# Optimization experiments

Hardware: AMD Instinct MI355X
Metric: run time of the kernel (lower is better)

The kernel has to match this reference:

```python
import jax, jax.numpy as jnp
import numpy as np


def _gelu(x):
    # torch nn.GELU default = exact erf form
    return jax.nn.gelu(x, approximate=False)


def setup_inputs() -> dict:
    key = jax.random.key(0)
    ks = jax.random.split(key, 10)
    B, C, S, L, Din, Dout = 32, 4, 256, 256, 256, 256
    return {
        "features": jax.random.normal(ks[0], (B, C, S, Din), jnp.float32),
        "features_mean": jax.random.normal(ks[1], (B, S, L), jnp.float32),
        "W1": jax.random.normal(ks[2], (1, 16), jnp.float32) * 0.5,
        "b1": jax.random.normal(ks[3], (16,), jnp.float32) * 0.1,
        "W2": jax.random.normal(ks[4], (16, 8), jnp.float32) * 0.25,
        "b2": jax.random.normal(ks[5], (8,), jnp.float32) * 0.1,
        "W3": jax.random.normal(ks[6], (8, 2), jnp.float32) * 0.35,
        "b3": jax.random.normal(ks[7], (2,), jnp.float32) * 0.1,
        "Wl": jax.random.normal(ks[8], (Din, Dout), jnp.float32) * (1.0 / np.sqrt(Din)),
        "bl": jax.random.normal(ks[9], (Dout,), jnp.float32) * 0.02,
    }


def reference(features, features_mean, W1, b1, W2, b2, W3, b3, Wl, bl):
    B, S, L = features_mean.shape
    # pairwise correlations -> [B, S*S, 1]
    corr = jnp.einsum('bsl,btl->bst', features_mean, features_mean).reshape(B, S * S, 1)
    # tiny pointwise MLP 1->16->8->2 with GELU, then log-softmax
    h = _gelu(corr @ W1 + b1)
    h = _gelu(h @ W2 + b2)
    logits = jax.nn.log_softmax(h @ W3 + b3, axis=-1)  # [B, S*S, 2]
    # gumbel-softmax, hard=True, tau=1 (straight-through; forward value is one-hot)
    u = jax.random.uniform(jax.random.key(42), logits.shape, logits.dtype, 1e-10, 1.0)
    g = -jnp.log(-jnp.log(u))
    y_soft = jax.nn.softmax(logits + g, axis=-1)
    y_hard = jax.nn.one_hot(jnp.argmax(y_soft, axis=-1), 2, dtype=y_soft.dtype)
    y = jax.lax.stop_gradient(y_hard - y_soft) + y_soft
    adj = y[..., 0].reshape(B, S, S)
    # mix in identity: a + (1 - a) * I (forces self-loops)
    eye = jnp.eye(S, dtype=adj.dtype)
    adj = adj + (1.0 - adj) * eye
    # degree (row) normalization
    adj = adj * (1.0 / jnp.sum(adj, axis=-1, keepdims=True))
    # propagate: [B,1,S,S] @ [B,C,S,Din]
    x = jnp.einsum('bst,bctd->bcsd', adj, features)
    return x @ Wl + bl
```

## Files before the change

### kernel.cpp

```cpp
#include <hip/hip_runtime.h>
#include <stdint.h>


#define TBL_INTERVALS 131072
#define TBL_MIN -128.0f
#define TBL_SCALE 512.0f
#define WL_CAP 131072u

typedef __attribute__((ext_vector_type(8))) short short8v;
typedef __attribute__((ext_vector_type(4))) short short4v;
typedef __attribute__((ext_vector_type(4))) float float4v;

__device__ __forceinline__ void threefry2x32(uint32_t x0, uint32_t x1,
                                             uint32_t& o0, uint32_t& o1) {
  const uint32_t ks0 = 0u;
  const uint32_t ks1 = 42u;
  const uint32_t ks2 = 0x1BD11BDAu ^ ks0 ^ ks1;
  const uint32_t ks[3] = {ks0, ks1, ks2};
  const uint32_t rot[2][4] = {{13u, 15u, 26u, 6u}, {17u, 29u, 16u, 24u}};
  x0 += ks0;
  x1 += ks1;
#pragma unroll
  for (int i = 0; i < 5; ++i) {
#pragma unroll
    for (int j = 0; j < 4; ++j) {
      const uint32_t r = rot[i & 1][j];
      x0 += x1;
      x1 = (x1 << r) | (x1 >> (32u - r));
      x1 ^= x0;
    }
    x0 += ks[(i + 1) % 3];
    x1 += ks[(i + 2) % 3] + (uint32_t)(i + 1);
  }
  o0 = x0;
  o1 = x1;
}

__device__ __forceinline__ float uniform_at(uint32_t j) {
  uint32_t o0, o1;
  threefry2x32(0u, j, o0, o1);
  const uint32_t bits = o0 ^ o1;
  uint32_t fb = (bits >> 9) | 0x3F800000u;
  float frac = __uint_as_float(fb) - 1.0f;
  return fmaxf(frac + 1e-10f, 1e-10f);
}

__device__ __forceinline__ double gumbel64_at(uint32_t j) {
  double t = -log((double)uniform_at(j));
  return -log(t);
}

__device__ __forceinline__ float gumbel32_at(uint32_t j) {
  float t = -logf(uniform_at(j));
  return -logf(t);
}

__device__ __forceinline__ double gelu_d(double x) {
  return 0.5 * x * (1.0 + erf(x * 0.70710678118654752440));
}

__device__ __forceinline__ float gelu_f(float x) {
  return 0.5f * x * (1.0f + erff(x * 0.70710678f));
}

__device__ __forceinline__ float mlp32(float corr, const float* __restrict__ W1,
                                       const float* __restrict__ b1,
                                       const float* __restrict__ W2,
                                       const float* __restrict__ b2,
                                       const float* __restrict__ W3,
                                       const float* __restrict__ b3) {
  float h1[16];
#pragma unroll
  for (int u = 0; u < 16; ++u) h1[u] = gelu_f(fmaf(corr, W1[u], b1[u]));
  float h2[8];
#pragma unroll
  for (int v = 0; v < 8; ++v) {
    float x = b2[v];
#pragma unroll
    for (int u = 0; u < 16; ++u) x = fmaf(h1[u], W2[u * 8 + v], x);
    h2[v] = gelu_f(x);
  }
  float l0 = b3[0], l1 = b3[1];
#pragma unroll
  for (int v = 0; v < 8; ++v) {
    l0 = fmaf(h2[v], W3[v * 2 + 0], l0);
    l1 = fmaf(h2[v], W3[v * 2 + 1], l1);
  }
  return l0 - l1;
}

__device__ __forceinline__ void split_bf16(float x, short& h, short& l) {
  uint32_t u = __float_as_uint(x);
  uint32_t hr = (u + 0x7FFFu + ((u >> 16) & 1u)) >> 16;
  float hf = __uint_as_float(hr << 16);
  float lo = x - hf;
  uint32_t v = __float_as_uint(lo);
  uint32_t lr = (v + 0x7FFFu + ((v >> 16) & 1u)) >> 16;
  h = (short)hr;
  l = (short)lr;
}

__device__ __forceinline__ short bf16_exact(float x) {
  return (short)(__float_as_uint(x) >> 16);
}

__global__ __launch_bounds__(256) void build_table_kernel(
    const float* __restrict__ W1, const float* __restrict__ b1,
    const float* __restrict__ W2, const float* __restrict__ b2,
    const float* __restrict__ W3, const float* __restrict__ b3,
    float* __restrict__ tbl) {
  const int i = blockIdx.x * 256 + threadIdx.x;
  if (i > TBL_INTERVALS) return;
  const float x = TBL_MIN + (float)i * (1.0f / TBL_SCALE);
  tbl[i] = mlp32(x, W1, b1, W2, b2, W3, b3);
}

__global__ void init_counter_kernel(uint32_t* __restrict__ c) { c[0] = 0u; }

__global__ __launch_bounds__(256) void corr_mfma_kernel(
    const float* __restrict__ fm, float* __restrict__ corr) {
  const int b = blockIdx.z;
  const float* base = fm + (size_t)b * 65536;
  const int row0 = blockIdx.y * 128;
  const int col0 = blockIdx.x * 128;

  __shared__ short Ah[128][40];
  __shared__ short Al[128][40];
  __shared__ short Bh[128][40];
  __shared__ short Bl[128][40];

  const int tid = threadIdx.x;
  const int w = tid >> 6;
  const int wr = (w >> 1) * 64;
  const int wc = (w & 1) * 64;
  const int lane = tid & 63;
  const int fcol = lane & 15;
  const int kg = lane >> 4;

  const int am = tid >> 1;
  const int ak = (tid & 1) * 16;

  float4v acc[4][4];
#pragma unroll
  for (int i = 0; i < 4; ++i)
#pragma unroll
    for (int j = 0; j < 4; ++j) acc[i][j] = (float4v)(0.0f);

  for (int k0 = 0; k0 < 256; k0 += 32) {
    float4 av[4], bv[4];
#pragma unroll
    for (int q = 0; q < 4; ++q) {
      av[q] = *(const float4*)(base + (size_t)(row0 + am) * 256 + k0 + ak + q * 4);
      bv[q] = *(const float4*)(base + (size_t)(col0 + am) * 256 + k0 + ak + q * 4);
    }

    __syncthreads();

    {
      short h[16], l[16];
#pragma unroll
      for (int q = 0; q < 4; ++q) {
        split_bf16(av[q].x, h[q * 4 + 0], l[q * 4 + 0]);
        split_bf16(av[q].y, h[q * 4 + 1], l[q * 4 + 1]);
        split_bf16(av[q].z, h[q * 4 + 2], l[q * 4 + 2]);
        split_bf16(av[q].w, h[q * 4 + 3], l[q * 4 + 3]);
      }
      *(short8v*)&Ah[am][ak] = *(short8v*)&h[0];
      *(short8v*)&Ah[am][ak + 8] = *(short8v*)&h[8];
      *(short8v*)&Al[am][ak] = *(short8v*)&l[0];
      *(short8v*)&Al[am][ak + 8] = *(short8v*)&l[8];
#pragma unroll
      for (int q = 0; q < 4; ++q) {
        split_bf16(bv[q].x, h[q * 4 + 0], l[q * 4 + 0]);
        split_bf16(bv[q].y, h[q * 4 + 1], l[q * 4 + 1]);
        split_bf16(bv[q].z, h[q * 4 + 2], l[q * 4 + 2]);
        split_bf16(bv[q].w, h[q * 4 + 3], l[q * 4 + 3]);
      }
      *(short8v*)&Bh[am][ak] = *(short8v*)&h[0];
      *(short8v*)&Bh[am][ak + 8] = *(short8v*)&h[8];
      *(short8v*)&Bl[am][ak] = *(short8v*)&l[0];
      *(short8v*)&Bl[am][ak + 8] = *(short8v*)&l[8];
    }
    __syncthreads();

    short8v afh[4], afl[4], bfh[4], bfl[4];
#pragma unroll
    for (int im = 0; im < 4; ++im) {
      afh[im] = *(const short8v*)&Ah[wr + im * 16 + fcol][kg * 8];
      afl[im] = *(const short8v*)&Al[wr + im * 16 + fcol][kg * 8];
    }
#pragma unroll
    for (int in = 0; in < 4; ++in) {
      bfh[in] = *(const short8v*)&Bh[wc + in * 16 + fcol][kg * 8];
      bfl[in] = *(const short8v*)&Bl[wc + in * 16 + fcol][kg * 8];
    }
#pragma unroll
    for (int im = 0; im < 4; ++im)
#pragma unroll
      for (int in = 0; in < 4; ++in) {
        acc[im][in] = __builtin_amdgcn_mfma_f32_16x16x32_bf16(
            afh[im], bfh[in], acc[im][in], 0, 0, 0);
        acc[im][in] = __builtin_amdgcn_mfma_f32_16x16x32_bf16(
            afh[im], bfl[in], acc[im][in], 0, 0, 0);
        acc[im][in] = __builtin_amdgcn_mfma_f32_16x16x32_bf16(
            afl[im], bfh[in], acc[im][in], 0, 0, 0);
        acc[im][in] = __builtin_amdgcn_mfma_f32_16x16x32_bf16(
            afl[im], bfl[in], acc[im][in], 0, 0, 0);
      }
  }

  float* Cb = corr + (size_t)b * 65536;
#pragma unroll
  for (int in = 0; in < 4; ++in) {
    const int col = col0 + wc + in * 16 + fcol;
#pragma unroll
    for (int im = 0; im < 4; ++im) {
      const int rbase = row0 + wr + im * 16 + kg * 4;
#pragma unroll
      for (int r = 0; r < 4; ++r)
        Cb[(size_t)(rbase + r) * 256 + col] = acc[im][in][r];
    }
  }
}

__global__ __launch_bounds__(256) void decide_fast_kernel(
    const float* __restrict__ corr, const float* __restrict__ tbl,
    float* __restrict__ adj_bin, uint32_t* __restrict__ counter,
    uint32_t* __restrict__ worklist) {
  const uint32_t flat = blockIdx.x * 256u + threadIdx.x;
  const int t = flat & 255;
  const int s = (flat >> 8) & 255;

  float a = 1.0f;
  bool pend = false;
  if (t != s) {
    const float cf = corr[flat];
    if (fabsf(cf) >= 127.0f) {
      pend = true;
      a = 0.0f;
    } else {
      const float xf = (cf - TBL_MIN) * TBL_SCALE;
      const int i = (int)xf;
      const float fr = xf - (float)i;
      const float t0v = tbl[i];
      const float t1v = tbl[i + 1];
      const float dt = t1v - t0v;
      const float dphi = fmaf(fr, dt, t0v);

      const float g0 = gumbel32_at(2u * flat);
      const float g1 = gumbel32_at(2u * flat + 1u);
      const float d = dphi - (g1 - g0);
      const float thr = fmaf(fabsf(dt), 0.3072f, 4e-4f);
      if (fabsf(d) >= thr) {
        a = (d >= 0.0f) ? 1.0f : 0.0f;
      } else {
        pend = true;
        a = 0.0f;
      }
    }
  }
  if (pend) {
    const uint32_t idx = atomicAdd(counter, 1u);
    if (idx < WL_CAP) worklist[idx] = flat;
  }
  adj_bin[flat] = a;
}

__global__ __launch_bounds__(256) void decide_exact_kernel(
    const float* __restrict__ fm, const uint32_t* __restrict__ counter,
    const uint32_t* __restrict__ worklist,
    const float* __restrict__ W1, const float* __restrict__ b1,
    const float* __restrict__ W2, const float* __restrict__ b2,
    const float* __restrict__ W3, const float* __restrict__ b3,
    float* __restrict__ adj_bin) {
  const uint32_t n = min(counter[0], WL_CAP);
  const uint32_t waveId = (blockIdx.x * 256u + threadIdx.x) >> 6;
  const uint32_t nWaves = (gridDim.x * 256u) >> 6;
  const int lane = threadIdx.x & 63;

  for (uint32_t it = waveId; it < n; it += nWaves) {
    const uint32_t flat = worklist[it];
    const uint32_t bb = flat >> 16;
    const uint32_t ss = (flat >> 8) & 255u;
    const uint32_t tt = flat & 255u;

    const float* S = fm + ((size_t)bb * 256 + ss) * 256;
    const float* T = fm + ((size_t)bb * 256 + tt) * 256;
    double p = 0.0;
#pragma unroll
    for (int q = 0; q < 4; ++q) {
      const int k = lane + q * 64;
      p += (double)S[k] * (double)T[k];
    }
#pragma unroll
    for (int off = 32; off; off >>= 1) p += __shfl_xor(p, off);
    const double acc = p;

    const double ga = gumbel64_at(2u * flat + (uint32_t)(lane & 1));

    const int u = lane & 15;
    const double h1 = gelu_d(acc * (double)W1[u] + (double)b1[u]);

    const int v = lane & 7;
    double sv = (double)b2[v];
#pragma unroll
    for (int uu = 0; uu < 16; ++uu) {
      const double h1u = __shfl(h1, uu);
      sv += h1u * (double)W2[uu * 8 + v];
    }
    const double h2 = gelu_d(sv);

    double l0 = (double)b3[0], l1 = (double)b3[1];
#pragma unroll
    for (int vv = 0; vv < 8; ++vv) {
      const double h2v = __shfl(h2, vv);
      l0 += h2v * (double)W3[vv * 2 + 0];
      l1 += h2v * (double)W3[vv * 2 + 1];
    }

    const double G0 = __shfl(ga, 0);
    const double G1 = __shfl(ga, 1);
    if (lane == 0) adj_bin[flat] = (l0 + G0 >= l1 + G1) ? 1.0f : 0.0f;
  }
}

__global__ __launch_bounds__(256) void rowscale_kernel(
    const float* __restrict__ adj_bin, float* __restrict__ rs) {
  const int row = blockIdx.x * 4 + (threadIdx.x >> 6);
  const int lane = threadIdx.x & 63;
  float4 v = ((const float4*)(adj_bin + (size_t)row * 256))[lane];
  float sum = v.x + v.y + v.z + v.w;
#pragma unroll
  for (int off = 32; off; off >>= 1) sum += __shfl_xor(sum, off);
  if (lane == 0) rs[row] = 1.0f / sum;
}

__global__ __launch_bounds__(256) void gemm_binA_kernel(
    const float* __restrict__ A, const float* __restrict__ B,
    const float* __restrict__ rs, float* __restrict__ C) {
  const int z = blockIdx.z;
  const float* Ab = A + (size_t)(z / 4) * 65536;
  const float* Bb = B + (size_t)z * 65536;
  const float* rsb = rs + (size_t)(z / 4) * 256;
  float* Cb = C + (size_t)z * 65536;

  const int row0 = blockIdx.y * 128;
  const int col0 = blockIdx.x * 128;

  __shared__ short Ah[128][40];
  __shared__ short Bh[128][40];
  __shared__ short Bl[128][40];

  const int tid = threadIdx.x;
  const int w = tid >> 6;
  const int wr = (w >> 1) * 64;
  const int wc = (w & 1) * 64;
  const int lane = tid & 63;
  const int fcol = lane & 15;
  const int kg = lane >> 4;

  const int am = tid >> 1;
  const int ak = (tid & 1) * 16;
  const int nq = (tid & 31) * 4;
  const int kb = (tid >> 5) * 4;

  float4v acc[4][4];
#pragma unroll
  for (int i = 0; i < 4; ++i)
#pragma unroll
    for (int j = 0; j < 4; ++j) acc[i][j] = (float4v)(0.0f);

  for (int k0 = 0; k0 < 256; k0 += 32) {
    float4 av[4];
#pragma unroll
    for (int q = 0; q < 4; ++q)
      av[q] = *(const float4*)(Ab + (size_t)(row0 + am) * 256 + k0 + ak + q * 4);
    float4 bv[4];
#pragma unroll
    for (int j = 0; j < 4; ++j)
      bv[j] = *(const float4*)(Bb + (size_t)(k0 + kb + j) * 256 + col0 + nq);

    __syncthreads();

    {
      short h[16];
#pragma unroll
      for (int q = 0; q < 4; ++q) {
        h[q * 4 + 0] = bf16_exact(av[q].x);
        h[q * 4 + 1] = bf16_exact(av[q].y);
        h[q * 4 + 2] = bf16_exact(av[q].z);
        h[q * 4 + 3] = bf16_exact(av[q].w);
      }
      *(short8v*)&Ah[am][ak] = *(short8v*)&h[0];
      *(short8v*)&Ah[am][ak + 8] = *(short8v*)&h[8];
    }
    {
      const float bm[4][4] = {{bv[0].x, bv[1].x, bv[2].x, bv[3].x},
                              {bv[0].y, bv[1].y, bv[2].y, bv[3].y},
                              {bv[0].z, bv[1].z, bv[2].z, bv[3].z},
                              {bv[0].w, bv[1].w, bv[2].w, bv[3].w}};
#pragma unroll
      for (int i = 0; i < 4; ++i) {
        short h[4], l[4];
#pragma unroll
        for (int j = 0; j < 4; ++j) split_bf16(bm[i][j], h[j], l[j]);
        *(short4v*)&Bh[nq + i][kb] = *(short4v*)&h[0];
        *(short4v*)&Bl[nq + i][kb] = *(short4v*)&l[0];
      }
    }
    __syncthreads();

    short8v afh[4], bfh[4], bfl[4];
#pragma unroll
    for (int im = 0; im < 4; ++im)
      afh[im] = *(const short8v*)&Ah[wr + im * 16 + fcol][kg * 8];
#pragma unroll
    for (int in = 0; in < 4; ++in) {
      bfh[in] = *(const short8v*)&Bh[wc + in * 16 + fcol][kg * 8];
      bfl[in] = *(const short8v*)&Bl[wc + in * 16 + fcol][kg * 8];
    }
#pragma unroll
    for (int im = 0; im < 4; ++im)
#pragma unroll
      for (int in = 0; in < 4; ++in) {
        acc[im][in] = __builtin_amdgcn_mfma_f32_16x16x32_bf16(
            afh[im], bfh[in], acc[im][in], 0, 0, 0);
        acc[im][in] = __builtin_amdgcn_mfma_f32_16x16x32_bf16(
            afh[im], bfl[in], acc[im][in], 0, 0, 0);
      }
  }

#pragma unroll
  for (int im = 0; im < 4; ++im) {
    const int rbase = row0 + wr + im * 16 + kg * 4;
    float rsv[4];
#pragma unroll
    for (int r = 0; r < 4; ++r) rsv[r] = rsb[rbase + r];
#pragma unroll
    for (int in = 0; in < 4; ++in) {
      const int col = col0 + wc + in * 16 + fcol;
#pragma unroll
      for (int r = 0; r < 4; ++r)
        Cb[(size_t)(rbase + r) * 256 + col] = acc[im][in][r] * rsv[r];
    }
  }
}

__global__ __launch_bounds__(256) void gemm_mfma_kernel(
    const float* __restrict__ A, const float* __restrict__ B,
    const float* __restrict__ bias, float* __restrict__ C) {
  const int z = blockIdx.z;
  const float* Ab = A + (size_t)z * 65536;
  const float* Bb = B;
  float* Cb = C + (size_t)z * 65536;

  const int row0 = blockIdx.y * 128;
  const int col0 = blockIdx.x * 128;

  __shared__ short Ah[128][40];
  __shared__ short Al[128][40];
  __shared__ short Bh[128][40];
  __shared__ short Bl[128][40];

  const int tid = threadIdx.x;
  const int w = tid >> 6;
  const int wr = (w >> 1) * 64;
  const int wc = (w & 1) * 64;
  const int lane = tid & 63;
  const int fcol = lane & 15;
  const int kg = lane >> 4;

  const int am = tid >> 1;
  const int ak = (tid & 1) * 16;
  const int nq = (tid & 31) * 4;
  const int kb = (tid >> 5) * 4;

  float4v acc[4][4];
#pragma unroll
  for (int i = 0; i < 4; ++i)
#pragma unroll
    for (int j = 0; j < 4; ++j) acc[i][j] = (float4v)(0.0f);

  for (int k0 = 0; k0 < 256; k0 += 32) {
    float4 av[4];
#pragma unroll
    for (int q = 0; q < 4; ++q)
      av[q] = *(const float4*)(Ab + (size_t)(row0 + am) * 256 + k0 + ak + q * 4);
    float4 bv[4];
#pragma unroll
    for (int j = 0; j < 4; ++j)
      bv[j] = *(const float4*)(Bb + (size_t)(k0 + kb + j) * 256 + col0 + nq);

    __syncthreads();

    {
      short h[16], l[16];
#pragma unroll
      for (int q = 0; q < 4; ++q) {
        split_bf16(av[q].x, h[q * 4 + 0], l[q * 4 + 0]);
        split_bf16(av[q].y, h[q * 4 + 1], l[q * 4 + 1]);
        split_bf16(av[q].z, h[q * 4 + 2], l[q * 4 + 2]);
        split_bf16(av[q].w, h[q * 4 + 3], l[q * 4 + 3]);
      }
      *(short8v*)&Ah[am][ak] = *(short8v*)&h[0];
      *(short8v*)&Ah[am][ak + 8] = *(short8v*)&h[8];
      *(short8v*)&Al[am][ak] = *(short8v*)&l[0];
      *(short8v*)&Al[am][ak + 8] = *(short8v*)&l[8];
    }
    {
      const float bm[4][4] = {{bv[0].x, bv[1].x, bv[2].x, bv[3].x},
                              {bv[0].y, bv[1].y, bv[2].y, bv[3].y},
                              {bv[0].z, bv[1].z, bv[2].z, bv[3].z},
                              {bv[0].w, bv[1].w, bv[2].w, bv[3].w}};
#pragma unroll
      for (int i = 0; i < 4; ++i) {
        short h[4], l[4];
#pragma unroll
        for (int j = 0; j < 4; ++j) split_bf16(bm[i][j], h[j], l[j]);
        *(short4v*)&Bh[nq + i][kb] = *(short4v*)&h[0];
        *(short4v*)&Bl[nq + i][kb] = *(short4v*)&l[0];
      }
    }
    __syncthreads();

    short8v afh[4], afl[4], bfh[4], bfl[4];
#pragma unroll
    for (int im = 0; im < 4; ++im) {
      afh[im] = *(const short8v*)&Ah[wr + im * 16 + fcol][kg * 8];
      afl[im] = *(const short8v*)&Al[wr + im * 16 + fcol][kg * 8];
    }
#pragma unroll
    for (int in = 0; in < 4; ++in) {
      bfh[in] = *(const short8v*)&Bh[wc + in * 16 + fcol][kg * 8];
      bfl[in] = *(const short8v*)&Bl[wc + in * 16 + fcol][kg * 8];
    }
#pragma unroll
    for (int im = 0; im < 4; ++im)
#pragma unroll
      for (int in = 0; in < 4; ++in) {
        acc[im][in] = __builtin_amdgcn_mfma_f32_16x16x32_bf16(
            afh[im], bfh[in], acc[im][in], 0, 0, 0);
        acc[im][in] = __builtin_amdgcn_mfma_f32_16x16x32_bf16(
            afh[im], bfl[in], acc[im][in], 0, 0, 0);
        acc[im][in] = __builtin_amdgcn_mfma_f32_16x16x32_bf16(
            afl[im], bfh[in], acc[im][in], 0, 0, 0);
      }
  }

#pragma unroll
  for (int in = 0; in < 4; ++in) {
    const int col = col0 + wc + in * 16 + fcol;
    const float bvx = bias[col];
#pragma unroll
    for (int im = 0; im < 4; ++im) {
      const int rbase = row0 + wr + im * 16 + kg * 4;
#pragma unroll
      for (int r = 0; r < 4; ++r)
        Cb[(size_t)(rbase + r) * 256 + col] = acc[im][in][r] + bvx;
    }
  }
}

extern "C" void kernel_launch(void* const* d_in, const int* in_sizes, int n_in,
                              void* d_out, int out_size, void* d_ws,
                              size_t ws_size, hipStream_t stream) {
  const float* features = (const float*)d_in[0];
  const float* fm       = (const float*)d_in[1];
  const float* W1 = (const float*)d_in[2];
  const float* b1 = (const float*)d_in[3];
  const float* W2 = (const float*)d_in[4];
  const float* b2 = (const float*)d_in[5];
  const float* W3 = (const float*)d_in[6];
  const float* b3 = (const float*)d_in[7];
  const float* Wl = (const float*)d_in[8];
  const float* bl = (const float*)d_in[9];
  float* out = (float*)d_out;

  char* ws = (char*)d_ws;
  float* tbl        = (float*)ws;
  float* rowscale   = (float*)(ws + 576u * 1024u);
  uint32_t* counter = (uint32_t*)(ws + 640u * 1024u);
  uint32_t* worklist = counter + 16;
  float* adj_bin    = (float*)(ws + 2u * 1024u * 1024u);
  float* corr       = (float*)(ws + 10800u * 1024u);
  float* X          = (float*)(ws + 10800u * 1024u);

  build_table_kernel<<<dim3(513), 256, 0, stream>>>(W1, b1, W2, b2, W3, b3,
                                                    tbl);
  init_counter_kernel<<<dim3(1), 1, 0, stream>>>(counter);
  corr_mfma_kernel<<<dim3(2, 2, 32), 256, 0, stream>>>(fm, corr);
  decide_fast_kernel<<<dim3(8192), 256, 0, stream>>>(corr, tbl, adj_bin,
                                                     counter, worklist);
  decide_exact_kernel<<<dim3(2048), 256, 0, stream>>>(fm, counter, worklist,
                                                      W1, b1, W2, b2, W3, b3,
                                                      adj_bin);
  rowscale_kernel<<<dim3(2048), 256, 0, stream>>>(adj_bin, rowscale);
  gemm_binA_kernel<<<dim3(2, 2, 128), 256, 0, stream>>>(adj_bin, features,
                                                        rowscale, X);
  gemm_mfma_kernel<<<dim3(2, 2, 128), 256, 0, stream>>>(X, Wl, bl, out);
}
```

Before: 97.18 us.

## Store adjacency as bf16, fuse row sums into decide kernels, drop helper launches

The binary adjacency is now written directly as bf16 bit patterns (ushort) rather than fp32, which halves that buffer's traffic and lets the propagation GEMM copy A tiles straight into shared memory without conversion. Row sums are computed in the fast decide kernel with a block reduction and corrected by atomic adds in the exact kernel, so the separate rowscale kernel goes away. The counter reset is folded into the table build kernel, removing another launch. In exchange it adds float atomics on row sums and a reciprocal in the GEMM epilogue.

```diff
diff --git a/kernel.cpp b/kernel.cpp
--- a/kernel.cpp
+++ b/kernel.cpp
@@ -100,22 +100,17 @@
   l = (short)lr;
 }
 
-__device__ __forceinline__ short bf16_exact(float x) {
-  return (short)(__float_as_uint(x) >> 16);
-}
-
 __global__ __launch_bounds__(256) void build_table_kernel(
     const float* __restrict__ W1, const float* __restrict__ b1,
     const float* __restrict__ W2, const float* __restrict__ b2,
     const float* __restrict__ W3, const float* __restrict__ b3,
-    float* __restrict__ tbl) {
+    float* __restrict__ tbl, uint32_t* __restrict__ counter) {
   const int i = blockIdx.x * 256 + threadIdx.x;
+  if (i == 0) counter[0] = 0u;
   if (i > TBL_INTERVALS) return;
   const float x = TBL_MIN + (float)i * (1.0f / TBL_SCALE);
   tbl[i] = mlp32(x, W1, b1, W2, b2, W3, b3);
 }
-
-__global__ void init_counter_kernel(uint32_t* __restrict__ c) { c[0] = 0u; }
 
 __global__ __launch_bounds__(256) void corr_mfma_kernel(
     const float* __restrict__ fm, float* __restrict__ corr) {
@@ -225,11 +220,11 @@
 
 __global__ __launch_bounds__(256) void decide_fast_kernel(
     const float* __restrict__ corr, const float* __restrict__ tbl,
-    float* __restrict__ adj_bin, uint32_t* __restrict__ counter,
-    uint32_t* __restrict__ worklist) {
+    unsigned short* __restrict__ adj_bin, uint32_t* __restrict__ counter,
+    uint32_t* __restrict__ worklist, float* __restrict__ rowsumF) {
   const uint32_t flat = blockIdx.x * 256u + threadIdx.x;
-  const int t = flat & 255;
-  const int s = (flat >> 8) & 255;
+  const int t = threadIdx.x;
+  const int s = blockIdx.x & 255;
 
   float a = 1.0f;
   bool pend = false;
@@ -263,7 +258,16 @@
     const uint32_t idx = atomicAdd(counter, 1u);
     if (idx < WL_CAP) worklist[idx] = flat;
   }
-  adj_bin[flat] = a;
+  adj_bin[flat] = (a == 1.0f) ? (unsigned short)0x3F80u : (unsigned short)0u;
+
+  float sum = a;
+#pragma unroll
+  for (int off = 32; off; off >>= 1) sum += __shfl_xor(sum, off);
+  __shared__ float red[4];
+  if ((threadIdx.x & 63) == 0) red[threadIdx.x >> 6] = sum;
+  __syncthreads();
+  if (threadIdx.x == 0)
+    rowsumF[blockIdx.x] = red[0] + red[1] + red[2] + red[3];
 }
 
 __global__ __launch_bounds__(256) void decide_exact_kernel(
@@ -272,7 +276,7 @@
     const float* __restrict__ W1, const float* __restrict__ b1,
     const float* __restrict__ W2, const float* __restrict__ b2,
     const float* __restrict__ W3, const float* __restrict__ b3,
-    float* __restrict__ adj_bin) {
+    unsigned short* __restrict__ adj_bin, float* __restrict__ rowsumF) {
   const uint32_t n = min(counter[0], WL_CAP);
   const uint32_t waveId = (blockIdx.x * 256u + threadIdx.x) >> 6;
   const uint32_t nWaves = (gridDim.x * 256u) >> 6;
@@ -320,28 +324,21 @@
 
     const double G0 = __shfl(ga, 0);
     const double G1 = __shfl(ga, 1);
-    if (lane == 0) adj_bin[flat] = (l0 + G0 >= l1 + G1) ? 1.0f : 0.0f;
-  }
-}
-
-__global__ __launch_bounds__(256) void rowscale_kernel(
-    const float* __restrict__ adj_bin, float* __restrict__ rs) {
-  const int row = blockIdx.x * 4 + (threadIdx.x >> 6);
-  const int lane = threadIdx.x & 63;
-  float4 v = ((const float4*)(adj_bin + (size_t)row * 256))[lane];
-  float sum = v.x + v.y + v.z + v.w;
-#pragma unroll
-  for (int off = 32; off; off >>= 1) sum += __shfl_xor(sum, off);
-  if (lane == 0) rs[row] = 1.0f / sum;
+    if (lane == 0) {
+      const bool one = (l0 + G0 >= l1 + G1);
+      adj_bin[flat] = one ? (unsigned short)0x3F80u : (unsigned short)0u;
+      if (one) atomicAdd(&rowsumF[flat >> 8], 1.0f);
+    }
+  }
 }
 
 __global__ __launch_bounds__(256) void gemm_binA_kernel(
-    const float* __restrict__ A, const float* __restrict__ B,
-    const float* __restrict__ rs, float* __restrict__ C) {
+    const unsigned short* __restrict__ A, const float* __restrict__ B,
+    const float* __restrict__ rowsumF, float* __restrict__ C) {
   const int z = blockIdx.z;
-  const float* Ab = A + (size_t)(z / 4) * 65536;
+  const unsigned short* Ab = A + (size_t)(z / 4) * 65536;
   const float* Bb = B + (size_t)z * 65536;
-  const float* rsb = rs + (size_t)(z / 4) * 256;
+  const float* rsb = rowsumF + (size_t)(z / 4) * 256;
   float* Cb = C + (size_t)z * 65536;
 
   const int row0 = blockIdx.y * 128;
@@ -371,10 +368,8 @@
     for (int j = 0; j < 4; ++j) acc[i][j] = (float4v)(0.0f);
 
   for (int k0 = 0; k0 < 256; k0 += 32) {
-    float4 av[4];
-#pragma unroll
-    for (int q = 0; q < 4; ++q)
-      av[q] = *(const float4*)(Ab + (size_t)(row0 + am) * 256 + k0 + ak + q * 4);
+    short8v a0 = *(const short8v*)(Ab + (size_t)(row0 + am) * 256 + k0 + ak);
+    short8v a1 = *(const short8v*)(Ab + (size_t)(row0 + am) * 256 + k0 + ak + 8);
     float4 bv[4];
 #pragma unroll
     for (int j = 0; j < 4; ++j)
@@ -382,18 +377,8 @@
 
     __syncthreads();
 
-    {
-      short h[16];
-#pragma unroll
-      for (int q = 0; q < 4; ++q) {
-        h[q * 4 + 0] = bf16_exact(av[q].x);
-        h[q * 4 + 1] = bf16_exact(av[q].y);
-        h[q * 4 + 2] = bf16_exact(av[q].z);
-        h[q * 4 + 3] = bf16_exact(av[q].w);
-      }
-      *(short8v*)&Ah[am][ak] = *(short8v*)&h[0];
-      *(short8v*)&Ah[am][ak + 8] = *(short8v*)&h[8];
-    }
+    *(short8v*)&Ah[am][ak] = a0;
+    *(short8v*)&Ah[am][ak + 8] = a1;
     {
       const float bm[4][4] = {{bv[0].x, bv[1].x, bv[2].x, bv[3].x},
                               {bv[0].y, bv[1].y, bv[2].y, bv[3].y},
@@ -435,7 +420,7 @@
     const int rbase = row0 + wr + im * 16 + kg * 4;
     float rsv[4];
 #pragma unroll
-    for (int r = 0; r < 4; ++r) rsv[r] = rsb[rbase + r];
+    for (int r = 0; r < 4; ++r) rsv[r] = 1.0f / rsb[rbase + r];
 #pragma unroll
     for (int in = 0; in < 4; ++in) {
       const int col = col0 + wc + in * 16 + fcol;
@@ -577,25 +562,23 @@
   float* out = (float*)d_out;
 
   char* ws = (char*)d_ws;
-  float* tbl        = (float*)ws;
-  float* rowscale   = (float*)(ws + 576u * 1024u);
-  uint32_t* counter = (uint32_t*)(ws + 640u * 1024u);
-  uint32_t* worklist = counter + 16;
-  float* adj_bin    = (float*)(ws + 2u * 1024u * 1024u);
-  float* corr       = (float*)(ws + 10800u * 1024u);
-  float* X          = (float*)(ws + 10800u * 1024u);
+  float* tbl          = (float*)ws;
+  float* rowsumF      = (float*)(ws + 576u * 1024u);
+  uint32_t* counter   = (uint32_t*)(ws + 640u * 1024u);
+  uint32_t* worklist  = counter + 16;
+  unsigned short* adj = (unsigned short*)(ws + 2u * 1024u * 1024u);
+  float* corr         = (float*)(ws + 10800u * 1024u);
+  float* X            = (float*)(ws + 10800u * 1024u);
 
   build_table_kernel<<<dim3(513), 256, 0, stream>>>(W1, b1, W2, b2, W3, b3,
-                                                    tbl);
-  init_counter_kernel<<<dim3(1), 1, 0, stream>>>(counter);
+                                                    tbl, counter);
   corr_mfma_kernel<<<dim3(2, 2, 32), 256, 0, stream>>>(fm, corr);
-  decide_fast_kernel<<<dim3(8192), 256, 0, stream>>>(corr, tbl, adj_bin,
-                                                     counter, worklist);
+  decide_fast_kernel<<<dim3(8192), 256, 0, stream>>>(corr, tbl, adj, counter,
+                                                     worklist, rowsumF);
   decide_exact_kernel<<<dim3(2048), 256, 0, stream>>>(fm, counter, worklist,
                                                       W1, b1, W2, b2, W3, b3,
-                                                      adj_bin);
-  rowscale_kernel<<<dim3(2048), 256, 0, stream>>>(adj_bin, rowscale);
-  gemm_binA_kernel<<<dim3(2, 2, 128), 256, 0, stream>>>(adj_bin, features,
-                                                        rowscale, X);
+                                                      adj, rowsumF);
+  gemm_binA_kernel<<<dim3(2, 2, 128), 256, 0, stream>>>(adj, features,
+                                                        rowsumF, X);
   gemm_mfma_kernel<<<dim3(2, 2, 128), 256, 0, stream>>>(X, Wl, bl, out);
 }
```

After: 94.08 us. 3.2% less time.
